# Kernel optimization log

Measured on AMD Instinct MI355X. Metric: run time of the kernel, lower is better.

Reference implementation:

```python
import jax, jax.numpy as jnp
import numpy as np
from jax.scipy.sparse.linalg import cg

SCALE = 8      # scaling_factor
CROP = 256     # crop_size
FEAT = 32      # per-branch feature channels
CG_ITERS = 100


def _conv(x, w, b):
    y = jax.lax.conv_general_dilated(x, w, (1, 1), 'SAME',
                                     dimension_numbers=('NCHW', 'OIHW', 'NCHW'))
    return y + b[None, :, None, None]


def _avgpool(x, r):
    B, C, H, W = x.shape
    return x.reshape(B, C, H // r, r, W // r, r).mean(axis=(3, 5))


def _up_adj(x, r):
    # adjoint of average-pool downsampling S: spread value / r^2 over the block
    return jnp.repeat(jnp.repeat(x, r, axis=2), r, axis=3) / (r * r)


def _features(guide, y_bicubic, gw1, gb1, gw2, gb2, sw1, sb1, sw2, sb2):
    g = _conv(jax.nn.relu(_conv(guide, gw1, gb1)), gw2, gb2)
    s = _conv(jax.nn.relu(_conv(y_bicubic, sw1, sb1)), sw2, sb2)
    return jnp.concatenate([g, s], axis=1)  # [B, 2*FEAT, H, W]


def _neighbor_affinity(f, mu, lam):
    # exp(-mu * ||f_i - f_j||^2) to the 4 grid neighbors, zero affinity at borders
    dv = jnp.sum((f[:, :, 1:, :] - f[:, :, :-1, :]) ** 2, axis=1)  # [B,H-1,W]
    dh = jnp.sum((f[:, :, :, 1:] - f[:, :, :, :-1]) ** 2, axis=1)  # [B,H,W-1]
    wv = jnp.exp(-mu * dv)
    wh = jnp.exp(-mu * dh)
    w_up = jnp.pad(wv, ((0, 0), (1, 0), (0, 0)))
    w_dn = jnp.pad(wv, ((0, 0), (0, 1), (0, 0)))
    w_lf = jnp.pad(wh, ((0, 0), (0, 0), (1, 0)))
    w_rt = jnp.pad(wh, ((0, 0), (0, 0), (0, 1)))
    deg = w_up + w_dn + w_lf + w_rt
    center = deg + lam  # diagonal of the system matrix (channel 4)
    return jnp.stack([w_up, w_dn, w_lf, w_rt, center], axis=1)  # [B,5,H,W]


def _graph_matvec(aff, mask_lr, lam, y):
    # A y = (D - W) y + lam * S^T M S y   (5-point graph Laplacian + LR data term)
    w_up, w_dn, w_lf, w_rt, center = (aff[:, i] for i in range(5))
    yy = y[:, 0]
    wy = (w_up * jnp.pad(yy[:, :-1, :], ((0, 0), (1, 0), (0, 0)))
          + w_dn * jnp.pad(yy[:, 1:, :], ((0, 0), (0, 1), (0, 0)))
          + w_lf * jnp.pad(yy[:, :, :-1], ((0, 0), (0, 0), (1, 0)))
          + w_rt * jnp.pad(yy[:, :, 1:], ((0, 0), (0, 0), (0, 1))))
    deg = center - lam
    lap = (deg * yy - wy)[:, None]
    data = lam * _up_adj(mask_lr * _avgpool(y, SCALE), SCALE)
    return lap + data


def setup_inputs() -> dict:
    key = jax.random.key(0)
    ks = jax.random.split(key, 20)
    B, H = 16, CROP
    r = SCALE
    w = lambda k, sh: jax.random.normal(k, sh, jnp.float32) * 0.05
    return {
        'guide': jax.random.normal(ks[0], (B, 3, H, H), jnp.float32),
        'source': jax.random.normal(ks[1], (B, 1, H // r, H // r), jnp.float32),
        'mask_lr': jnp.ones((B, 1, H // r, H // r), jnp.float32),
        'y_bicubic': jax.random.normal(ks[2], (B, 1, H, H), jnp.float32),
        # feature extractor (guide branch + source branch)
        'gw1': w(ks[3], (FEAT, 3, 3, 3)), 'gb1': jnp.zeros((FEAT,), jnp.float32),
        'gw2': w(ks[4], (FEAT, FEAT, 3, 3)), 'gb2': jnp.zeros((FEAT,), jnp.float32),
        'sw1': w(ks[5], (FEAT, 1, 3, 3)), 'sb1': jnp.zeros((FEAT,), jnp.float32),
        'sw2': w(ks[6], (FEAT, FEAT, 3, 3)), 'sb2': jnp.zeros((FEAT,), jnp.float32),
        # var_conv: VarEstimateModule(in=4, out=1, k=3)
        'vw1': w(ks[7], (FEAT, 4, 3, 3)), 'vb1': jnp.zeros((FEAT,), jnp.float32),
        'vw2': w(ks[8], (FEAT, FEAT, 3, 3)), 'vb2': jnp.zeros((FEAT,), jnp.float32),
        'vw3': w(ks[9], (1, FEAT, 3, 3)), 'vb3': jnp.zeros((1,), jnp.float32),
        # learned scalars (stored as log, as in the torch module)
        'log_lambda': jnp.log(jnp.array([1.0], jnp.float32)),
        'log_mu': jnp.log(jnp.array([0.1], jnp.float32)),
    }


def reference(guide, source, mask_lr, y_bicubic,
              gw1, gb1, gw2, gb2, sw1, sb1, sw2, sb2,
              vw1, vb1, vw2, vb2, vw3, vb3,
              log_lambda, log_mu):
    mu = jnp.exp(log_mu)[0]
    lam = jnp.exp(log_lambda)[0]
    # variance head on cat([guide, y_bicubic])
    v = jnp.concatenate([guide, y_bicubic], axis=1)
    v = jax.nn.relu(_conv(v, vw1, vb1))
    v = jax.nn.relu(_conv(v, vw2, vb2))
    var = _conv(v, vw3, vb3)
    # pixel affinities from multi-modal features
    feats = _features(guide, y_bicubic, gw1, gb1, gw2, gb2, sw1, sb1, sw2, sb2)
    aff = _neighbor_affinity(feats, mu, lam)
    # graph-regularised SR: solve (L + lam S^T M S) y = lam S^T (M source) by CG
    b = lam * _up_adj(mask_lr * source, SCALE)
    matvec = lambda y: _graph_matvec(aff, mask_lr, lam, y)
    y_pred, _ = cg(matvec, b, x0=y_bicubic, maxiter=CG_ITERS, tol=1e-6)
    return y_pred, var, aff
```

## Files before the change

### kernel.cpp

```cpp
#include <hip/hip_runtime.h>
#include <hip/hip_bf16.h>

typedef __hip_bfloat16 bf16;
typedef __attribute__((ext_vector_type(8))) short short8;
typedef __attribute__((ext_vector_type(4))) float f32x4;

#define NB 16
#define PLANE (256*256)

static __device__ __forceinline__ short f2bf(float v){
    __hip_bfloat16 h = __float2bfloat16(v);
    short s; __builtin_memcpy(&s, &h, 2); return s;
}
static __device__ __forceinline__ float bf2f(short s){
    union { unsigned u; float f; } cv;
    cv.u = ((unsigned)(unsigned short)s) << 16; return cv.f;
}

static __device__ __forceinline__ void  stg_ag(float* p, float v){
    __hip_atomic_store(p, v, __ATOMIC_RELAXED, __HIP_MEMORY_SCOPE_AGENT);
}
static __device__ __forceinline__ float ldg_ag(const float* p){
    return __hip_atomic_load(p, __ATOMIC_RELAXED, __HIP_MEMORY_SCOPE_AGENT);
}
static __device__ __forceinline__ void stg4_ag(float* p, f32x4 v){
    asm volatile("global_store_dwordx4 %0, %1, off sc0 sc1" :: "v"(p), "v"(v) : "memory");
}
static __device__ __forceinline__ f32x4 ldg4_ag(const float* p){
    f32x4 r;
    asm volatile("global_load_dwordx4 %0, %1, off sc0 sc1\n\ts_waitcnt vmcnt(0)"
                 : "=v"(r) : "v"(p) : "memory");
    return r;
}

template<int CIN, int SPLIT, bool RELU>
__global__ __launch_bounds__(256)
void conv3x3_first(const float* __restrict__ in, const float* __restrict__ in2,
                   const float* __restrict__ wgt, const float* __restrict__ bias,
                   bf16* __restrict__ out)
{
    __shared__ float s_in[CIN][18][18];
    __shared__ float s_w[CIN*9*32];
    const int n  = blockIdx.z;
    const int ty0 = blockIdx.y * 16, tx0 = blockIdx.x * 16;
    const int tid = threadIdx.x;

    for (int idx = tid; idx < CIN*9*32; idx += 256) {
        int co = idx & 31; int rest = idx >> 5;
        s_w[idx] = wgt[(co*CIN + rest/9)*9 + rest%9];
    }
    for (int idx = tid; idx < CIN*18*18; idx += 256) {
        int ci = idx / (18*18); int rr = idx % (18*18);
        int yy = rr / 18, xx = rr % 18;
        int y = ty0 + yy - 1, x = tx0 + xx - 1;
        float v = 0.f;
        if (y >= 0 && y < 256 && x >= 0 && x < 256) {
            if (ci < SPLIT) v = in [((size_t)(n*SPLIT + ci)*256 + y)*256 + x];
            else            v = in2[((size_t)(n*(CIN-SPLIT) + (ci-SPLIT))*256 + y)*256 + x];
        }
        s_in[ci][yy][xx] = v;
    }
    __syncthreads();

    const int ty = tid >> 4, tx = tid & 15;
    float acc[32];
    #pragma unroll
    for (int co = 0; co < 32; co++) acc[co] = bias[co];

    #pragma unroll
    for (int ci = 0; ci < CIN; ci++) {
        #pragma unroll
        for (int ky = 0; ky < 3; ky++)
        #pragma unroll
        for (int kx = 0; kx < 3; kx++) {
            float v = s_in[ci][ty+ky][tx+kx];
            const float* wp = &s_w[(ci*9 + ky*3 + kx)*32];
            #pragma unroll
            for (int co = 0; co < 32; co++) acc[co] = fmaf(v, wp[co], acc[co]);
        }
    }
    const int y = ty0 + ty, x = tx0 + tx;
    size_t base = (((size_t)n*256 + y)*256 + x)*32;
    #pragma unroll
    for (int c = 0; c < 32; c += 8) {
        short8 vv;
        #pragma unroll
        for (int j = 0; j < 8; j++) {
            float v = acc[c+j];
            if (RELU) v = fmaxf(v, 0.f);
            vv[j] = f2bf(v);
        }
        *(short8*)((short*)out + base + c) = vv;
    }
}

__global__ __launch_bounds__(256)
void wrepack3(const float* __restrict__ a, const float* __restrict__ b,
              const float* __restrict__ c,
              bf16* __restrict__ oa, bf16* __restrict__ ob, bf16* __restrict__ oc)
{
    int j = blockIdx.x*256 + threadIdx.x;
    if (j >= 3*9216) return;
    int set = j / 9216, r = j % 9216;
    int tap = r >> 10, rem = r & 1023, co = rem >> 5, ci = rem & 31;
    const float* src = (set == 0) ? a : (set == 1) ? b : c;
    bf16* dst = (set == 0) ? oa : (set == 1) ? ob : oc;
    dst[r] = __float2bfloat16(src[(co*32 + ci)*9 + tap]);
}

template<bool RELU>
__global__ __launch_bounds__(256)
void conv3x3_mfma(const bf16* __restrict__ in, const bf16* __restrict__ wpk,
                  const float* __restrict__ bias, bf16* __restrict__ out)
{
    __shared__ __align__(16) short s_a[4*2640];
    const int tid = threadIdx.x;
    const int lane = tid & 63, wid = tid >> 6;
    const int m = lane & 15, quad = lane >> 4, k0 = quad*8;
    const int n  = blockIdx.z;
    const int x0 = blockIdx.x * 16;
    const int y0 = blockIdx.y * 16;

    const short* inp = (const short*)in + (size_t)n*PLANE*32;
    short* outp = (short*)out + (size_t)n*PLANE*32;

    for (int c = tid; c < 1296; c += 256) {
        int q = c & 3, px = c >> 2;
        int yy = px / 18, xx = px - yy*18;
        int gy = y0 + yy - 1, gx = x0 + xx - 1;
        short8 v = {0,0,0,0,0,0,0,0};
        if ((unsigned)gy < 256u && (unsigned)gx < 256u)
            v = *(const short8*)(inp + ((size_t)(gy*256 + gx))*32 + q*8);
        *(short8*)(s_a + q*2640 + (yy*18 + xx)*8) = v;
    }

    const short* wp = (const short*)wpk;
    short8 bw[2][9];
    #pragma unroll
    for (int g = 0; g < 2; g++)
        #pragma unroll
        for (int tap = 0; tap < 9; tap++)
            bw[g][tap] = *(const short8*)(wp + ((tap*32 + g*16 + m)*32 + k0));
    const float b0 = bias[m], b1 = bias[16 + m];
    __syncthreads();

    const short* sa = s_a + quad*2640;
    #pragma unroll
    for (int r = 0; r < 4; r++) {
        const int lr = wid*4 + r;
        f32x4 acc0 = { b0, b0, b0, b0 };
        f32x4 acc1 = { b1, b1, b1, b1 };
        #pragma unroll
        for (int ky = 0; ky < 3; ky++)
        #pragma unroll
        for (int kx = 0; kx < 3; kx++) {
            short8 a = *(const short8*)(sa + ((lr+ky)*18 + (m+kx))*8);
            acc0 = __builtin_amdgcn_mfma_f32_16x16x32_bf16(a, bw[0][ky*3+kx], acc0, 0, 0, 0);
            acc1 = __builtin_amdgcn_mfma_f32_16x16x32_bf16(a, bw[1][ky*3+kx], acc1, 0, 0, 0);
        }
        const int y = y0 + lr;
        #pragma unroll
        for (int reg = 0; reg < 4; reg++) {
            int px = x0 + quad*4 + reg;
            size_t idx = ((size_t)y*256 + px)*32;
            float v0 = acc0[reg], v1 = acc1[reg];
            if (RELU) { v0 = fmaxf(v0, 0.f); v1 = fmaxf(v1, 0.f); }
            outp[idx + m]      = f2bf(v0);
            outp[idx + 16 + m] = f2bf(v1);
        }
    }
}

template<bool ACCUM>
__global__ __launch_bounds__(256, 2)
void conv3x3_mfma_dvdh(const bf16* __restrict__ in, const bf16* __restrict__ wpk,
                       const float* __restrict__ bias,
                       float* __restrict__ dv, float* __restrict__ dh)
{
    __shared__ __align__(16) short s_a[4*2896];
    __shared__ __align__(16) short s_f[17*17*40];
    const int tid = threadIdx.x;
    const int lane = tid & 63, wid = tid >> 6;
    const int m = lane & 15, quad = lane >> 4, k0 = quad*8;
    const int n  = blockIdx.z;
    const int x0 = blockIdx.x * 16;
    const int y0 = blockIdx.y * 16;

    const short* inp = (const short*)in + (size_t)n*PLANE*32;

    for (int c = tid; c < 1444; c += 256) {
        int q = c & 3, px = c >> 2;
        int yy = px / 19, xx = px - yy*19;
        int gy = y0 + yy - 1, gx = x0 + xx - 1;
        short8 v = {0,0,0,0,0,0,0,0};
        if ((unsigned)gy < 256u && (unsigned)gx < 256u)
            v = *(const short8*)(inp + ((size_t)(gy*256 + gx))*32 + q*8);
        *(short8*)(s_a + q*2896 + (yy*19 + xx)*8) = v;
    }

    const short* wp = (const short*)wpk;
    short8 bw[2][9];
    #pragma unroll
    for (int g = 0; g < 2; g++)
        #pragma unroll
        for (int tap = 0; tap < 9; tap++)
            bw[g][tap] = *(const short8*)(wp + ((tap*32 + g*16 + m)*32 + k0));
    const float b0 = bias[m], b1 = bias[16 + m];
    __syncthreads();

    const short* sa = s_a + quad*2896;

    for (int ru = 0; ru < 5; ru++) {
        const int yl = wid + 4*ru;
        if (yl > 16) break;
        f32x4 acc0 = { b0, b0, b0, b0 };
        f32x4 acc1 = { b1, b1, b1, b1 };
        #pragma unroll
        for (int ky = 0; ky < 3; ky++)
        #pragma unroll
        for (int kx = 0; kx < 3; kx++) {
            short8 a = *(const short8*)(sa + ((yl+ky)*19 + (kx+m))*8);
            acc0 = __builtin_amdgcn_mfma_f32_16x16x32_bf16(a, bw[0][ky*3+kx], acc0, 0, 0, 0);
            acc1 = __builtin_amdgcn_mfma_f32_16x16x32_bf16(a, bw[1][ky*3+kx], acc1, 0, 0, 0);
        }
        #pragma unroll
        for (int reg = 0; reg < 4; reg++) {
            int c = quad*4 + reg;
            short* fp = s_f + (yl*17 + c)*40;
            fp[m]      = f2bf(acc0[reg]);
            fp[16 + m] = f2bf(acc1[reg]);
        }
    }

    for (int ru = 0; ru < 4; ru++) {
        const int yl = wid + 4*ru;
        f32x4 acc0 = { b0, b0, b0, b0 };
        f32x4 acc1 = { b1, b1, b1, b1 };
        #pragma unroll
        for (int ky = 0; ky < 3; ky++)
        #pragma unroll
        for (int kx = 0; kx < 3; kx++) {
            int col = 16 + kx + m; if (col > 18) col = 18;
            short8 a = *(const short8*)(sa + ((yl+ky)*19 + col)*8);
            acc0 = __builtin_amdgcn_mfma_f32_16x16x32_bf16(a, bw[0][ky*3+kx], acc0, 0, 0, 0);
            acc1 = __builtin_amdgcn_mfma_f32_16x16x32_bf16(a, bw[1][ky*3+kx], acc1, 0, 0, 0);
        }
        if (quad == 0) {
            short* fp = s_f + (yl*17 + 16)*40;
            fp[m]      = f2bf(acc0[0]);
            fp[16 + m] = f2bf(acc1[0]);
        }
    }
    __syncthreads();

    const int ty = tid >> 4, tx = tid & 15;
    const int i = y0 + ty, j = x0 + tx;
    const short8* pc = (const short8*)(s_f + (ty*17 + tx)*40);
    const short8* pr = (j < 255) ? (const short8*)(s_f + (ty*17 + tx + 1)*40) : pc;
    const short8* pd = (i < 255) ? (const short8*)(s_f + ((ty+1)*17 + tx)*40) : pc;
    float adv = 0.f, adh = 0.f;
    #pragma unroll
    for (int c4 = 0; c4 < 4; c4++) {
        short8 sc = pc[c4], sr = pr[c4], sd = pd[c4];
        #pragma unroll
        for (int e = 0; e < 8; e++) {
            float fc = bf2f(sc[e]);
            float d1 = bf2f(sr[e]) - fc;
            float d2 = bf2f(sd[e]) - fc;
            adh = fmaf(d1, d1, adh);
            adv = fmaf(d2, d2, adv);
        }
    }
    int o = (n*256 + i)*256 + j;
    if (ACCUM) { dv[o] += adv; dh[o] += adh; }
    else       { dv[o]  = adv; dh[o]  = adh; }
}

__global__ __launch_bounds__(256)
void conv3x3_last(const bf16* __restrict__ in, const float* __restrict__ wgt,
                  const float* __restrict__ bias, float* __restrict__ out)
{
    __shared__ float s_w[288];
    int tid = threadIdx.x;
    for (int i = tid; i < 288; i += 256) s_w[i] = wgt[i];
    __syncthreads();
    int gid = blockIdx.x*256 + tid;
    int n = gid >> 16, h = (gid >> 8) & 255, w = gid & 255;
    const short* inp = (const short*)in + (size_t)n*PLANE*32;
    float sum = bias[0];
    #pragma unroll
    for (int ky = 0; ky < 3; ky++) {
        int yy = h + ky - 1;
        if ((unsigned)yy >= 256u) continue;
        #pragma unroll
        for (int kx = 0; kx < 3; kx++) {
            int xx = w + kx - 1;
            if ((unsigned)xx >= 256u) continue;
            const short8* pp = (const short8*)(inp + ((size_t)yy*256 + xx)*32);
            int tap = ky*3 + kx;
            #pragma unroll
            for (int c4 = 0; c4 < 4; c4++) {
                short8 v = pp[c4];
                #pragma unroll
                for (int j = 0; j < 8; j++)
                    sum = fmaf(bf2f(v[j]), s_w[(c4*8+j)*9 + tap], sum);
            }
        }
    }
    out[gid] = sum;
}

__global__ __launch_bounds__(256)
void aff2_kernel(const float* __restrict__ dv, const float* __restrict__ dh,
                 const float* __restrict__ llam, const float* __restrict__ lmu,
                 unsigned* __restrict__ wvh, float* __restrict__ aff)
{
    int bid = blockIdx.x;
    int n = bid >> 8, h = bid & 255, w = threadIdx.x;
    float mu = expf(lmu[0]), lam = expf(llam[0]);
    int rb = (n*256 + h)*256 + w;
    float wvv = (h < 255) ? expf(-mu * dv[rb]) : 0.f;
    float whv = (w < 255) ? expf(-mu * dh[rb]) : 0.f;
    unsigned pv = (unsigned)(unsigned short)f2bf(wvv);
    unsigned ph = (unsigned)(unsigned short)f2bf(whv);
    wvh[rb] = pv | (ph << 16);
    float w_up = (h > 0) ? expf(-mu * dv[rb - 256]) : 0.f;
    float w_lf = (w > 0) ? expf(-mu * dh[rb - 1])   : 0.f;
    float ctr  = w_up + wvv + w_lf + whv + lam;
    float* a = aff + ((size_t)n*5)*PLANE + h*256 + w;
    a[0]        = w_up;
    a[PLANE]    = wvv;
    a[2*PLANE]  = w_lf;
    a[3*PLANE]  = whv;
    a[4*PLANE]  = ctr;
}

__global__ __launch_bounds__(256, 2)
void cg_persist(const unsigned* __restrict__ wvh, const float* __restrict__ mask,
                const float* __restrict__ src, const float* __restrict__ ybic,
                const float* __restrict__ llam, float* __restrict__ xout,
                float* __restrict__ ebuf0, float* __restrict__ ebuf1,
                float* __restrict__ part4, float* __restrict__ res4)
{
    __shared__ float s_pn[66][34];
    __shared__ float s_part[256], s_bs[32];
    __shared__ float s_w3[12];
    __shared__ __align__(16) float s_g[16];

    const int tid = threadIdx.x;
    const int wb = blockIdx.x;
    const int n = wb >> 5, t = wb & 31;
    const int tyo = (t >> 3) * 64, txo = (t & 7) * 32;
    const int tx = tid & 31, tyb = tid >> 5;
    const int w = txo + tx;
    const float lam = expf(llam[0]);
    const bool is_leader = ((wb & 127) == 0);

    const unsigned* wn = wvh + (size_t)n*PLANE;
    const float* ybn = ybic + (size_t)n*PLANE;

    int idx[8];
    unsigned wc[8], wu[8], wl[8];
    float c1[8], rhs[8];
    #pragma unroll
    for (int i = 0; i < 8; i++) {
        int hhi = tyo + tyb + 8*i;
        idx[i] = hhi*256 + w;
        wc[i] = wn[idx[i]];
        wu[i] = (hhi > 0) ? wn[idx[i]-256] : 0u;
        wl[i] = (w > 0)   ? wn[idx[i]-1]   : 0u;
        int bi = n*1024 + (hhi>>3)*32 + (w>>3);
        float mv = mask[bi];
        c1[i]  = lam*mv*(1.f/4096.f);
        rhs[i] = lam*mv*src[bi]*(1.f/64.f);
    }

    const bool hthr = (tid < 192);
    int hy = 0, hx = 0; bool hin = false; int nb = 0, eoff = 0;
    if (hthr) {
        if      (tid < 32)  { hy = tyo - 1;         hx = txo + tid;
                              nb = wb - 8; eoff = 32 + tid; }
        else if (tid < 64)  { hy = tyo + 64;        hx = txo + (tid-32);
                              nb = wb + 8; eoff = tid - 32; }
        else if (tid < 128) { hy = tyo + (tid-64);  hx = txo - 1;
                              nb = wb - 1; eoff = 128 + (tid-64); }
        else                { hy = tyo + (tid-128); hx = txo + 32;
                              nb = wb + 1; eoff = 64 + (tid-128); }
        hin = (hy >= 0 && hy < 256 && hx >= 0 && hx < 256);
    }
    const int hsy = hy - tyo + 1, hsx = hx - txo + 1;

    #define POOL_BLOCK() do { \
        __syncthreads(); \
        { int segrow_ = tid >> 2, segcol_ = tid & 3; \
          const float* rw_ = &s_pn[1 + segrow_][1 + segcol_*8]; \
          s_part[tid] = rw_[0]+rw_[1]+rw_[2]+rw_[3]+rw_[4]+rw_[5]+rw_[6]+rw_[7]; } \
        __syncthreads(); \
        if (tid < 32) { int brow_ = tid >> 2, bcol_ = tid & 3; float s_ = 0.f; \
          _Pragma("unroll") \
          for (int rr_ = 0; rr_ < 8; rr_++) s_ += s_part[(brow_*8 + rr_)*4 + bcol_]; \
          s_bs[tid] = s_; } \
        __syncthreads(); \
    } while (0)

    #define PUBLISH_E(arr, ebase) do { \
        float* eb_ = (ebase) + (size_t)wb*192; \
        if (tyb == 0) stg_ag(eb_ + tx, arr[0]); \
        if (tyb == 7) stg_ag(eb_ + 32 + tx, arr[7]); \
        if (tx == 0) { _Pragma("unroll") \
            for (int i_ = 0; i_ < 8; i_++) stg_ag(eb_ + 64 + tyb + 8*i_, arr[i_]); } \
        if (tx == 31){ _Pragma("unroll") \
            for (int i_ = 0; i_ < 8; i_++) stg_ag(eb_ + 128 + tyb + 8*i_, arr[i_]); } \
    } while (0)

    auto matvec = [&](int i) -> float {
        int yy = 1 + tyb + 8*i, xx = 1 + tx;
        float wvd = bf2f((short)(wc[i] & 0xffff));
        float whr = bf2f((short)(wc[i] >> 16));
        float wvu = bf2f((short)(wu[i] & 0xffff));
        float whl = bf2f((short)(wl[i] >> 16));
        float s = wvu*s_pn[yy-1][xx] + wvd*s_pn[yy+1][xx]
                + whl*s_pn[yy][xx-1] + whr*s_pn[yy][xx+1];
        float deg = wvu+wvd+whl+whr;
        return deg*s_pn[yy][xx] - s + c1[i]*s_bs[i*4 + (tx>>3)];
    };

    auto publish_red = [&](unsigned seq, float va, float vb, float vc){
        #pragma unroll
        for (int o = 32; o > 0; o >>= 1) {
            va += __shfl_down(va, o, 64);
            vb += __shfl_down(vb, o, 64);
            vc += __shfl_down(vc, o, 64);
        }
        asm volatile("s_waitcnt vmcnt(0)" ::: "memory");
        __syncthreads();
        if ((tid & 63) == 0) { int wv = tid >> 6; s_w3[wv*3]=va; s_w3[wv*3+1]=vb; s_w3[wv*3+2]=vc; }
        __syncthreads();
        if (tid == 0) {
            f32x4 pk;
            pk[0] = s_w3[0]+s_w3[3]+s_w3[6]+s_w3[9];
            pk[1] = s_w3[1]+s_w3[4]+s_w3[7]+s_w3[10];
            pk[2] = s_w3[2]+s_w3[5]+s_w3[8]+s_w3[11];
            pk[3] = __uint_as_float(seq);
            stg4_ag(part4 + (size_t)((seq & 1)*512 + wb)*4, pk);
        }
    };

    float o0, o1, o2;
    auto allred = [&](unsigned seq){
        float* resp = res4 + (size_t)(seq & 1)*64;
        if (is_leader && tid < 64) {
            const float* pl = part4 + (size_t)(seq & 1)*2048;
            const float* p0 = pl + (size_t)(wb + 2*tid)*4;
            f32x4 a0 = ldg4_ag(p0);
            while (__float_as_uint(a0[3]) < seq) { __builtin_amdgcn_s_sleep(1); a0 = ldg4_ag(p0); }
            f32x4 a1 = ldg4_ag(p0 + 4);
            while (__float_as_uint(a1[3]) < seq) { __builtin_amdgcn_s_sleep(1); a1 = ldg4_ag(p0 + 4); }
            float pa = a0[0] + a1[0];
            float pb = a0[1] + a1[1];
            float pc = a0[2] + a1[2];
            #pragma unroll
            for (int o = 32; o > 0; o >>= 1) {
                pa += __shfl_down(pa, o, 64);
                pb += __shfl_down(pb, o, 64);
                pc += __shfl_down(pc, o, 64);
            }
            if (tid == 0) {
                f32x4 rk; rk[0] = pa; rk[1] = pb; rk[2] = pc; rk[3] = __uint_as_float(seq);
                stg4_ag(resp + (wb >> 7)*16, rk);
            }
        }
        if (tid < 4) {
            const float* rl = resp + tid*16;
            f32x4 g = ldg4_ag(rl);
            while (__float_as_uint(g[3]) < seq) { __builtin_amdgcn_s_sleep(2); g = ldg4_ag(rl); }
            *(f32x4*)&s_g[tid*4] = g;
        }
        __syncthreads();
        o0 = ((s_g[0]+s_g[4])+s_g[8])+s_g[12];
        o1 = ((s_g[1]+s_g[5])+s_g[9])+s_g[13];
        o2 = ((s_g[2]+s_g[6])+s_g[10])+s_g[14];
    };

    float xv[8], rv[8], pv[8], apv[8];
    float rh = 0.f, phh = 0.f;

    #pragma unroll
    for (int i = 0; i < 8; i++) {
        xv[i] = ybn[idx[i]];
        s_pn[1 + tyb + 8*i][1 + tx] = xv[i];
    }
    if (hthr) s_pn[hsy][hsx] = hin ? ybn[hy*256 + hx] : 0.f;
    POOL_BLOCK();
    float g0t = 0.f;
    #pragma unroll
    for (int i = 0; i < 8; i++) {
        float ax = matvec(i);
        float r0 = rhs[i] - ax;
        rv[i] = r0; pv[i] = r0;
        g0t += r0*r0;
    }
    PUBLISH_E(pv, ebuf1);
    publish_red(1u, 0.f, 0.f, 0.f);
    allred(1u);

    {
        float hv = 0.f;
        if (hthr && hin) hv = ldg_ag(ebuf1 + (size_t)nb*192 + eoff);
        if (hthr) { rh = hv; phh = hv; s_pn[hsy][hsx] = phh; }
        #pragma unroll
        for (int i = 0; i < 8; i++) s_pn[1 + tyb + 8*i][1 + tx] = pv[i];
        POOL_BLOCK();
        float pap = 0.f, apap = 0.f;
        #pragma unroll
        for (int i = 0; i < 8; i++) {
            float ap = matvec(i);
            apv[i] = ap;
            pap  += pv[i]*ap;
            apap += ap*ap;
        }
        PUBLISH_E(apv, ebuf0);
        publish_red(2u, g0t, pap, apap);
    }

    for (int k = 1; k <= 99; k++) {
        float* ebR = ((k+1) & 1) ? ebuf1 : ebuf0;
        float* ebW = ((k+2) & 1) ? ebuf1 : ebuf0;

        allred((unsigned)(k + 1));
        float alpha = o0 / o1;
        float beta  = (alpha*alpha*o2 - o0) / o0;

        float hv = 0.f;
        if (hthr && hin) hv = ldg_ag(ebR + (size_t)nb*192 + eoff);

        float gsum = 0.f;
        #pragma unroll
        for (int i = 0; i < 8; i++) {
            float rN = fmaf(-alpha, apv[i], rv[i]);
            xv[i] = fmaf(alpha, pv[i], xv[i]);
            float pN = fmaf(beta, pv[i], rN);
            rv[i] = rN; pv[i] = pN;
            gsum += rN*rN;
            s_pn[1 + tyb + 8*i][1 + tx] = pN;
        }
        if (hthr) {
            rh  = fmaf(-alpha, hv, rh);
            phh = fmaf(beta, phh, rh);
            s_pn[hsy][hsx] = phh;
        }
        POOL_BLOCK();
        float pap = 0.f, apap = 0.f;
        #pragma unroll
        for (int i = 0; i < 8; i++) {
            float ap = matvec(i);
            apv[i] = ap;
            pap  += pv[i]*ap;
            apap += ap*ap;
        }
        PUBLISH_E(apv, ebW);
        publish_red((unsigned)(k + 2), gsum, pap, apap);
    }

    allred(101u);
    float alphaT = o0 / o1;
    float* xn = xout + (size_t)n*PLANE;
    #pragma unroll
    for (int i = 0; i < 8; i++) xn[idx[i]] = fmaf(alphaT, pv[i], xv[i]);

    #undef POOL_BLOCK
    #undef PUBLISH_E
}

extern "C" void kernel_launch(void* const* d_in, const int* in_sizes, int n_in,
                              void* d_out, int out_size, void* d_ws, size_t ws_size,
                              hipStream_t stream)
{
    (void)in_sizes; (void)n_in; (void)out_size; (void)ws_size;
    const float* guide = (const float*)d_in[0];
    const float* source= (const float*)d_in[1];
    const float* mask  = (const float*)d_in[2];
    const float* ybic  = (const float*)d_in[3];
    const float* gw1 = (const float*)d_in[4];  const float* gb1 = (const float*)d_in[5];
    const float* gw2 = (const float*)d_in[6];  const float* gb2 = (const float*)d_in[7];
    const float* sw1 = (const float*)d_in[8];  const float* sb1 = (const float*)d_in[9];
    const float* sw2 = (const float*)d_in[10]; const float* sb2 = (const float*)d_in[11];
    const float* vw1 = (const float*)d_in[12]; const float* vb1 = (const float*)d_in[13];
    const float* vw2 = (const float*)d_in[14]; const float* vb2 = (const float*)d_in[15];
    const float* vw3 = (const float*)d_in[16]; const float* vb3 = (const float*)d_in[17];
    const float* llam = (const float*)d_in[18];
    const float* lmu  = (const float*)d_in[19];

    float* out     = (float*)d_out;
    float* x_out   = out;
    float* var_out = out + 1048576;
    float* aff_out = out + 2097152;

    char* ws = (char*)d_ws;
    float*    res4  = (float*)ws;
    float*    part4 = (float*)(ws + 4096);
    bf16*     wpk1  = (bf16*)(ws + 24576);
    bf16*     wpk2  = (bf16*)(ws + 43008);
    bf16*     wpk3  = (bf16*)(ws + 61440);
    unsigned* wvh   = (unsigned*)(ws + 131072);
    char*     A     = ws + 131072 + (size_t)NB*PLANE*4;
    bf16*  tmp1 = (bf16*)(A);
    bf16*  tmp2 = (bf16*)(A + (size_t)NB*32*PLANE*2);
    float* dv   = (float*)(A + (size_t)NB*32*PLANE*4);
    float* dh   = (float*)(A + (size_t)NB*32*PLANE*4 + (size_t)NB*PLANE*4);
    float* ebuf0 = (float*)A;
    float* ebuf1 = (float*)(A + (size_t)512*192*4);

    dim3 cgrid(16, 16, NB);

    hipMemsetAsync(ws, 0, 20480, stream);

    wrepack3<<<108,256,0,stream>>>(gw2, sw2, vw2, wpk1, wpk2, wpk3);

    conv3x3_first<3,3,true><<<cgrid,256,0,stream>>>(guide, guide, gw1, gb1, tmp1);
    conv3x3_mfma_dvdh<false><<<cgrid,256,0,stream>>>(tmp1, wpk1, gb2, dv, dh);
    conv3x3_first<1,1,true><<<cgrid,256,0,stream>>>(ybic, ybic, sw1, sb1, tmp1);
    conv3x3_mfma_dvdh<true><<<cgrid,256,0,stream>>>(tmp1, wpk2, sb2, dv, dh);
    aff2_kernel<<<4096,256,0,stream>>>(dv, dh, llam, lmu, wvh, aff_out);
    conv3x3_first<4,3,true><<<cgrid,256,0,stream>>>(guide, ybic, vw1, vb1, tmp1);
    conv3x3_mfma<true><<<cgrid,256,0,stream>>>(tmp1, wpk3, vb2, tmp2);
    conv3x3_last<<<4096,256,0,stream>>>(tmp2, vw3, vb3, var_out);

    cg_persist<<<512,256,0,stream>>>(wvh, mask, source, ybic, llam, x_out,
                                     ebuf0, ebuf1, part4, res4);
}
```

Measured before the change: 894.5 us.

## Fuse both feature-branch second convs, dv/dh, and affinity into one kernel

Both feature branches' second 3x3 convolutions, the squared-difference sums and the exp affinity computation now run in one kernel, with dv/dh kept in shared memory. This removes the global dv/dh round trips, the read-modify-write accumulation pass and the separate aff2 launch. In exchange, each tile recomputes a halo of 18x18 conv outputs (from 17x17) so the up/left neighbours are available locally, and shared-memory use per block rises. The first-layer outputs of the two branches now go to separate buffers.

Result: slower. 986.0 us (+10.2%).

```diff
diff --git a/kernel.cpp b/kernel.cpp
--- a/kernel.cpp
+++ b/kernel.cpp
@@ -171,14 +171,17 @@
     }
 }
 
-template<bool ACCUM>
 __global__ __launch_bounds__(256, 2)
-void conv3x3_mfma_dvdh(const bf16* __restrict__ in, const bf16* __restrict__ wpk,
-                       const float* __restrict__ bias,
-                       float* __restrict__ dv, float* __restrict__ dh)
+void featfuse(const bf16* __restrict__ ing, const bf16* __restrict__ ins,
+              const bf16* __restrict__ wpk1, const float* __restrict__ gb2,
+              const bf16* __restrict__ wpk2, const float* __restrict__ sb2,
+              const float* __restrict__ llam, const float* __restrict__ lmu,
+              unsigned* __restrict__ wvh, float* __restrict__ aff)
 {
-    __shared__ __align__(16) short s_a[4*2896];
-    __shared__ __align__(16) short s_f[17*17*40];
+    __shared__ __align__(16) short s_a[4*3248];
+    __shared__ __align__(16) short s_f[18*18*40];
+    __shared__ float s_dv[17][17], s_dh[17][17];
+
     const int tid = threadIdx.x;
     const int lane = tid & 63, wid = tid >> 6;
     const int m = lane & 15, quad = lane >> 4, k0 = quad*8;
@@ -186,94 +189,127 @@
     const int x0 = blockIdx.x * 16;
     const int y0 = blockIdx.y * 16;
 
-    const short* inp = (const short*)in + (size_t)n*PLANE*32;
-
-    for (int c = tid; c < 1444; c += 256) {
-        int q = c & 3, px = c >> 2;
-        int yy = px / 19, xx = px - yy*19;
-        int gy = y0 + yy - 1, gx = x0 + xx - 1;
-        short8 v = {0,0,0,0,0,0,0,0};
-        if ((unsigned)gy < 256u && (unsigned)gx < 256u)
-            v = *(const short8*)(inp + ((size_t)(gy*256 + gx))*32 + q*8);
-        *(short8*)(s_a + q*2896 + (yy*19 + xx)*8) = v;
-    }
-
-    const short* wp = (const short*)wpk;
-    short8 bw[2][9];
-    #pragma unroll
-    for (int g = 0; g < 2; g++)
-        #pragma unroll
-        for (int tap = 0; tap < 9; tap++)
-            bw[g][tap] = *(const short8*)(wp + ((tap*32 + g*16 + m)*32 + k0));
-    const float b0 = bias[m], b1 = bias[16 + m];
-    __syncthreads();
-
-    const short* sa = s_a + quad*2896;
-
-    for (int ru = 0; ru < 5; ru++) {
-        const int yl = wid + 4*ru;
-        if (yl > 16) break;
-        f32x4 acc0 = { b0, b0, b0, b0 };
-        f32x4 acc1 = { b1, b1, b1, b1 };
-        #pragma unroll
-        for (int ky = 0; ky < 3; ky++)
-        #pragma unroll
-        for (int kx = 0; kx < 3; kx++) {
-            short8 a = *(const short8*)(sa + ((yl+ky)*19 + (kx+m))*8);
-            acc0 = __builtin_amdgcn_mfma_f32_16x16x32_bf16(a, bw[0][ky*3+kx], acc0, 0, 0, 0);
-            acc1 = __builtin_amdgcn_mfma_f32_16x16x32_bf16(a, bw[1][ky*3+kx], acc1, 0, 0, 0);
-        }
-        #pragma unroll
-        for (int reg = 0; reg < 4; reg++) {
-            int c = quad*4 + reg;
-            short* fp = s_f + (yl*17 + c)*40;
-            fp[m]      = f2bf(acc0[reg]);
-            fp[16 + m] = f2bf(acc1[reg]);
-        }
-    }
-
-    for (int ru = 0; ru < 4; ru++) {
-        const int yl = wid + 4*ru;
-        f32x4 acc0 = { b0, b0, b0, b0 };
-        f32x4 acc1 = { b1, b1, b1, b1 };
-        #pragma unroll
-        for (int ky = 0; ky < 3; ky++)
-        #pragma unroll
-        for (int kx = 0; kx < 3; kx++) {
-            int col = 16 + kx + m; if (col > 18) col = 18;
-            short8 a = *(const short8*)(sa + ((yl+ky)*19 + col)*8);
-            acc0 = __builtin_amdgcn_mfma_f32_16x16x32_bf16(a, bw[0][ky*3+kx], acc0, 0, 0, 0);
-            acc1 = __builtin_amdgcn_mfma_f32_16x16x32_bf16(a, bw[1][ky*3+kx], acc1, 0, 0, 0);
-        }
-        if (quad == 0) {
-            short* fp = s_f + (yl*17 + 16)*40;
-            fp[m]      = f2bf(acc0[0]);
-            fp[16 + m] = f2bf(acc1[0]);
-        }
-    }
+    auto stage20 = [&](const short* inp){
+        for (int c = tid; c < 1600; c += 256) {
+            int q = c & 3, px = c >> 2;
+            int yy = px / 20, xx = px - yy*20;
+            int gy = y0 + yy - 2, gx = x0 + xx - 2;
+            short8 v = {0,0,0,0,0,0,0,0};
+            if ((unsigned)gy < 256u && (unsigned)gx < 256u)
+                v = *(const short8*)(inp + ((size_t)(gy*256 + gx))*32 + q*8);
+            *(short8*)(s_a + q*3248 + (yy*20 + xx)*8) = v;
+        }
+    };
+
+    auto conv2 = [&](const bf16* wpk, const float* bias){
+        const short* wp = (const short*)wpk;
+        short8 bw[2][9];
+        #pragma unroll
+        for (int g = 0; g < 2; g++)
+            #pragma unroll
+            for (int tap = 0; tap < 9; tap++)
+                bw[g][tap] = *(const short8*)(wp + ((tap*32 + g*16 + m)*32 + k0));
+        const float b0 = bias[m], b1 = bias[16 + m];
+        const short* sa = s_a + quad*3248;
+
+        for (int ly = wid; ly < 18; ly += 4) {
+            f32x4 acc0 = { b0, b0, b0, b0 };
+            f32x4 acc1 = { b1, b1, b1, b1 };
+            #pragma unroll
+            for (int ky = 0; ky < 3; ky++)
+            #pragma unroll
+            for (int kx = 0; kx < 3; kx++) {
+                short8 a = *(const short8*)(sa + ((ly+ky)*20 + (m+kx))*8);
+                acc0 = __builtin_amdgcn_mfma_f32_16x16x32_bf16(a, bw[0][ky*3+kx], acc0, 0, 0, 0);
+                acc1 = __builtin_amdgcn_mfma_f32_16x16x32_bf16(a, bw[1][ky*3+kx], acc1, 0, 0, 0);
+            }
+            #pragma unroll
+            for (int reg = 0; reg < 4; reg++) {
+                int lx = quad*4 + reg;
+                short* fp = s_f + (ly*18 + lx)*40;
+                fp[m]      = f2bf(acc0[reg]);
+                fp[16 + m] = f2bf(acc1[reg]);
+            }
+            f32x4 e0 = { b0, b0, b0, b0 };
+            f32x4 e1 = { b1, b1, b1, b1 };
+            #pragma unroll
+            for (int ky = 0; ky < 3; ky++)
+            #pragma unroll
+            for (int kx = 0; kx < 3; kx++) {
+                int col = 16 + m + kx; if (col > 19) col = 19;
+                short8 a = *(const short8*)(sa + ((ly+ky)*20 + col)*8);
+                e0 = __builtin_amdgcn_mfma_f32_16x16x32_bf16(a, bw[0][ky*3+kx], e0, 0, 0, 0);
+                e1 = __builtin_amdgcn_mfma_f32_16x16x32_bf16(a, bw[1][ky*3+kx], e1, 0, 0, 0);
+            }
+            if (quad == 0) {
+                #pragma unroll
+                for (int reg = 0; reg < 2; reg++) {
+                    short* fp = s_f + (ly*18 + 16 + reg)*40;
+                    fp[m]      = f2bf(e0[reg]);
+                    fp[16 + m] = f2bf(e1[reg]);
+                }
+            }
+        }
+    };
+
+    auto dvdh = [&](bool accum){
+        for (int p = tid; p < 289; p += 256) {
+            int li = p / 17, lj = p % 17;
+            int gi = y0 - 1 + li, gj = x0 - 1 + lj;
+            const short8* pc = (const short8*)(s_f + (li*18 + lj)*40);
+            const short8* pr = (gj < 255) ? (const short8*)(s_f + (li*18 + lj + 1)*40) : pc;
+            const short8* pd = (gi < 255) ? (const short8*)(s_f + ((li+1)*18 + lj)*40) : pc;
+            float adv = 0.f, adh = 0.f;
+            #pragma unroll
+            for (int c4 = 0; c4 < 4; c4++) {
+                short8 sc = pc[c4], sr = pr[c4], sd = pd[c4];
+                #pragma unroll
+                for (int e = 0; e < 8; e++) {
+                    float fc = bf2f(sc[e]);
+                    float d1 = bf2f(sr[e]) - fc;
+                    float d2 = bf2f(sd[e]) - fc;
+                    adh = fmaf(d1, d1, adh);
+                    adv = fmaf(d2, d2, adv);
+                }
+            }
+            if (accum) { s_dv[li][lj] += adv; s_dh[li][lj] += adh; }
+            else       { s_dv[li][lj]  = adv; s_dh[li][lj]  = adh; }
+        }
+    };
+
+    const short* ipg = (const short*)ing + (size_t)n*PLANE*32;
+    const short* ips = (const short*)ins + (size_t)n*PLANE*32;
+
+    stage20(ipg);
+    __syncthreads();
+    conv2(wpk1, gb2);
+    __syncthreads();
+    dvdh(false);
+    stage20(ips);
+    __syncthreads();
+    conv2(wpk2, sb2);
+    __syncthreads();
+    dvdh(true);
     __syncthreads();
 
     const int ty = tid >> 4, tx = tid & 15;
-    const int i = y0 + ty, j = x0 + tx;
-    const short8* pc = (const short8*)(s_f + (ty*17 + tx)*40);
-    const short8* pr = (j < 255) ? (const short8*)(s_f + (ty*17 + tx + 1)*40) : pc;
-    const short8* pd = (i < 255) ? (const short8*)(s_f + ((ty+1)*17 + tx)*40) : pc;
-    float adv = 0.f, adh = 0.f;
-    #pragma unroll
-    for (int c4 = 0; c4 < 4; c4++) {
-        short8 sc = pc[c4], sr = pr[c4], sd = pd[c4];
-        #pragma unroll
-        for (int e = 0; e < 8; e++) {
-            float fc = bf2f(sc[e]);
-            float d1 = bf2f(sr[e]) - fc;
-            float d2 = bf2f(sd[e]) - fc;
-            adh = fmaf(d1, d1, adh);
-            adv = fmaf(d2, d2, adv);
-        }
-    }
-    int o = (n*256 + i)*256 + j;
-    if (ACCUM) { dv[o] += adv; dh[o] += adh; }
-    else       { dv[o]  = adv; dh[o]  = adh; }
+    const int h = y0 + ty, w = x0 + tx;
+    const float mu = expf(lmu[0]), lam = expf(llam[0]);
+    int rb = (n*256 + h)*256 + w;
+    float wvv = (h < 255) ? expf(-mu * s_dv[ty+1][tx+1]) : 0.f;
+    float whv = (w < 255) ? expf(-mu * s_dh[ty+1][tx+1]) : 0.f;
+    unsigned pv = (unsigned)(unsigned short)f2bf(wvv);
+    unsigned ph = (unsigned)(unsigned short)f2bf(whv);
+    wvh[rb] = pv | (ph << 16);
+    float w_up = (h > 0) ? expf(-mu * s_dv[ty][tx+1]) : 0.f;
+    float w_lf = (w > 0) ? expf(-mu * s_dh[ty+1][tx]) : 0.f;
+    float ctr  = w_up + wvv + w_lf + whv + lam;
+    float* a = aff + ((size_t)n*5)*PLANE + h*256 + w;
+    a[0]        = w_up;
+    a[PLANE]    = wvv;
+    a[2*PLANE]  = w_lf;
+    a[3*PLANE]  = whv;
+    a[4*PLANE]  = ctr;
 }
 
 __global__ __launch_bounds__(256)
@@ -308,31 +344,6 @@
         }
     }
     out[gid] = sum;
-}
-
-__global__ __launch_bounds__(256)
-void aff2_kernel(const float* __restrict__ dv, const float* __restrict__ dh,
-                 const float* __restrict__ llam, const float* __restrict__ lmu,
-                 unsigned* __restrict__ wvh, float* __restrict__ aff)
-{
-    int bid = blockIdx.x;
-    int n = bid >> 8, h = bid & 255, w = threadIdx.x;
-    float mu = expf(lmu[0]), lam = expf(llam[0]);
-    int rb = (n*256 + h)*256 + w;
-    float wvv = (h < 255) ? expf(-mu * dv[rb]) : 0.f;
-    float whv = (w < 255) ? expf(-mu * dh[rb]) : 0.f;
-    unsigned pv = (unsigned)(unsigned short)f2bf(wvv);
-    unsigned ph = (unsigned)(unsigned short)f2bf(whv);
-    wvh[rb] = pv | (ph << 16);
-    float w_up = (h > 0) ? expf(-mu * dv[rb - 256]) : 0.f;
-    float w_lf = (w > 0) ? expf(-mu * dh[rb - 1])   : 0.f;
-    float ctr  = w_up + wvv + w_lf + whv + lam;
-    float* a = aff + ((size_t)n*5)*PLANE + h*256 + w;
-    a[0]        = w_up;
-    a[PLANE]    = wvv;
-    a[2*PLANE]  = w_lf;
-    a[3*PLANE]  = whv;
-    a[4*PLANE]  = ctr;
 }
 
 __global__ __launch_bounds__(256, 2)
@@ -604,10 +615,8 @@
     bf16*     wpk3  = (bf16*)(ws + 61440);
     unsigned* wvh   = (unsigned*)(ws + 131072);
     char*     A     = ws + 131072 + (size_t)NB*PLANE*4;
-    bf16*  tmp1 = (bf16*)(A);
-    bf16*  tmp2 = (bf16*)(A + (size_t)NB*32*PLANE*2);
-    float* dv   = (float*)(A + (size_t)NB*32*PLANE*4);
-    float* dh   = (float*)(A + (size_t)NB*32*PLANE*4 + (size_t)NB*PLANE*4);
+    bf16*  tmpA = (bf16*)(A);
+    bf16*  tmpB = (bf16*)(A + (size_t)NB*32*PLANE*2);
     float* ebuf0 = (float*)A;
     float* ebuf1 = (float*)(A + (size_t)512*192*4);
 
@@ -617,14 +626,13 @@
 
     wrepack3<<<108,256,0,stream>>>(gw2, sw2, vw2, wpk1, wpk2, wpk3);
 
-    conv3x3_first<3,3,true><<<cgrid,256,0,stream>>>(guide, guide, gw1, gb1, tmp1);
-    conv3x3_mfma_dvdh<false><<<cgrid,256,0,stream>>>(tmp1, wpk1, gb2, dv, dh);
-    conv3x3_first<1,1,true><<<cgrid,256,0,stream>>>(ybic, ybic, sw1, sb1, tmp1);
-    conv3x3_mfma_dvdh<true><<<cgrid,256,0,stream>>>(tmp1, wpk2, sb2, dv, dh);
-    aff2_kernel<<<4096,256,0,stream>>>(dv, dh, llam, lmu, wvh, aff_out);
-    conv3x3_first<4,3,true><<<cgrid,256,0,stream>>>(guide, ybic, vw1, vb1, tmp1);
-    conv3x3_mfma<true><<<cgrid,256,0,stream>>>(tmp1, wpk3, vb2, tmp2);
-    conv3x3_last<<<4096,256,0,stream>>>(tmp2, vw3, vb3, var_out);
+    conv3x3_first<3,3,true><<<cgrid,256,0,stream>>>(guide, guide, gw1, gb1, tmpA);
+    conv3x3_first<1,1,true><<<cgrid,256,0,stream>>>(ybic, ybic, sw1, sb1, tmpB);
+    featfuse<<<cgrid,256,0,stream>>>(tmpA, tmpB, wpk1, gb2, wpk2, sb2,
+                                     llam, lmu, wvh, aff_out);
+    conv3x3_first<4,3,true><<<cgrid,256,0,stream>>>(guide, ybic, vw1, vb1, tmpA);
+    conv3x3_mfma<true><<<cgrid,256,0,stream>>>(tmpA, wpk3, vb2, tmpB);
+    conv3x3_last<<<4096,256,0,stream>>>(tmpB, vw3, vb3, var_out);
 
     cg_persist<<<512,256,0,stream>>>(wvh, mask, source, ybic, llam, x_out,
                                      ebuf0, ebuf1, part4, res4);
```

## Merge guide/source branch convs into shared launches and fuse variance conv1 with affinity

Applied to the files above, without the earlier changes.

Runs the guide and source first-layer convs in one launch, and their MFMA second-layer convs with dv/dh reduction in one launch, using a doubled z-grid. The two branches' dv/dh contributions now combine through atomicAdd into a buffer cleared beforehand, instead of a write pass followed by an accumulate pass. The variance head's first conv shares one launch with the affinity kernel through block-index partitioning. This cuts the number of launches and serialization points and gives each launch more blocks, at the cost of an extra memset and float atomics.

Measured after the change: 876.0 us. -2.1%, faster.

```diff
diff --git a/kernel.cpp b/kernel.cpp
--- a/kernel.cpp
+++ b/kernel.cpp
@@ -33,24 +33,19 @@
     return r;
 }
 
-template<int CIN, int SPLIT, bool RELU>
-__global__ __launch_bounds__(256)
-void conv3x3_first(const float* __restrict__ in, const float* __restrict__ in2,
-                   const float* __restrict__ wgt, const float* __restrict__ bias,
-                   bf16* __restrict__ out)
-{
-    __shared__ float s_in[CIN][18][18];
-    __shared__ float s_w[CIN*9*32];
-    const int n  = blockIdx.z;
-    const int ty0 = blockIdx.y * 16, tx0 = blockIdx.x * 16;
-    const int tid = threadIdx.x;
-
+template<int CIN, int SPLIT>
+static __device__ __forceinline__ void conv1_body(
+    const float* __restrict__ in, const float* __restrict__ in2,
+    const float* __restrict__ wgt, const float* __restrict__ bias,
+    bf16* __restrict__ out, float* s_in, float* s_w,
+    int n, int ty0, int tx0, int tid)
+{
     for (int idx = tid; idx < CIN*9*32; idx += 256) {
         int co = idx & 31; int rest = idx >> 5;
         s_w[idx] = wgt[(co*CIN + rest/9)*9 + rest%9];
     }
     for (int idx = tid; idx < CIN*18*18; idx += 256) {
-        int ci = idx / (18*18); int rr = idx % (18*18);
+        int ci = idx / 324; int rr = idx % 324;
         int yy = rr / 18, xx = rr % 18;
         int y = ty0 + yy - 1, x = tx0 + xx - 1;
         float v = 0.f;
@@ -58,7 +53,7 @@
             if (ci < SPLIT) v = in [((size_t)(n*SPLIT + ci)*256 + y)*256 + x];
             else            v = in2[((size_t)(n*(CIN-SPLIT) + (ci-SPLIT))*256 + y)*256 + x];
         }
-        s_in[ci][yy][xx] = v;
+        s_in[ci*324 + yy*18 + xx] = v;
     }
     __syncthreads();
 
@@ -73,7 +68,7 @@
         for (int ky = 0; ky < 3; ky++)
         #pragma unroll
         for (int kx = 0; kx < 3; kx++) {
-            float v = s_in[ci][ty+ky][tx+kx];
+            float v = s_in[ci*324 + (ty+ky)*18 + (tx+kx)];
             const float* wp = &s_w[(ci*9 + ky*3 + kx)*32];
             #pragma unroll
             for (int co = 0; co < 32; co++) acc[co] = fmaf(v, wp[co], acc[co]);
@@ -85,13 +80,27 @@
     for (int c = 0; c < 32; c += 8) {
         short8 vv;
         #pragma unroll
-        for (int j = 0; j < 8; j++) {
-            float v = acc[c+j];
-            if (RELU) v = fmaxf(v, 0.f);
-            vv[j] = f2bf(v);
-        }
+        for (int j = 0; j < 8; j++)
+            vv[j] = f2bf(fmaxf(acc[c+j], 0.f));
         *(short8*)((short*)out + base + c) = vv;
     }
+}
+
+__global__ __launch_bounds__(256)
+void conv1_gs(const float* __restrict__ guide, const float* __restrict__ ybic,
+              const float* __restrict__ gw1, const float* __restrict__ gb1,
+              const float* __restrict__ sw1, const float* __restrict__ sb1,
+              bf16* __restrict__ outg, bf16* __restrict__ outs)
+{
+    __shared__ float s_in[3*324];
+    __shared__ float s_w[3*9*32];
+    const int zz = blockIdx.z;
+    const int br = zz >> 4, n = zz & 15;
+    const int ty0 = blockIdx.y * 16, tx0 = blockIdx.x * 16;
+    if (br == 0)
+        conv1_body<3,3>(guide, guide, gw1, gb1, outg, s_in, s_w, n, ty0, tx0, threadIdx.x);
+    else
+        conv1_body<1,1>(ybic, ybic, sw1, sb1, outs, s_in, s_w, n, ty0, tx0, threadIdx.x);
 }
 
 __global__ __launch_bounds__(256)
@@ -171,20 +180,25 @@
     }
 }
 
-template<bool ACCUM>
 __global__ __launch_bounds__(256, 2)
-void conv3x3_mfma_dvdh(const bf16* __restrict__ in, const bf16* __restrict__ wpk,
-                       const float* __restrict__ bias,
-                       float* __restrict__ dv, float* __restrict__ dh)
+void conv2gs_dvdh(const bf16* __restrict__ ing, const bf16* __restrict__ ins,
+                  const bf16* __restrict__ wpk1, const float* __restrict__ gb2,
+                  const bf16* __restrict__ wpk2, const float* __restrict__ sb2,
+                  float* __restrict__ dv, float* __restrict__ dh)
 {
     __shared__ __align__(16) short s_a[4*2896];
     __shared__ __align__(16) short s_f[17*17*40];
     const int tid = threadIdx.x;
     const int lane = tid & 63, wid = tid >> 6;
     const int m = lane & 15, quad = lane >> 4, k0 = quad*8;
-    const int n  = blockIdx.z;
+    const int zz = blockIdx.z;
+    const int br = zz >> 4, n = zz & 15;
     const int x0 = blockIdx.x * 16;
     const int y0 = blockIdx.y * 16;
+
+    const bf16* in = br ? ins : ing;
+    const bf16* wpk = br ? wpk2 : wpk1;
+    const float* bias = br ? sb2 : gb2;
 
     const short* inp = (const short*)in + (size_t)n*PLANE*32;
 
@@ -272,8 +286,8 @@
         }
     }
     int o = (n*256 + i)*256 + j;
-    if (ACCUM) { dv[o] += adv; dh[o] += adh; }
-    else       { dv[o]  = adv; dh[o]  = adh; }
+    atomicAdd(&dv[o], adv);
+    atomicAdd(&dh[o], adh);
 }
 
 __global__ __launch_bounds__(256)
@@ -311,11 +325,23 @@
 }
 
 __global__ __launch_bounds__(256)
-void aff2_kernel(const float* __restrict__ dv, const float* __restrict__ dh,
-                 const float* __restrict__ llam, const float* __restrict__ lmu,
-                 unsigned* __restrict__ wvh, float* __restrict__ aff)
-{
-    int bid = blockIdx.x;
+void conv1v_aff(const float* __restrict__ guide, const float* __restrict__ ybic,
+                const float* __restrict__ vw1, const float* __restrict__ vb1,
+                bf16* __restrict__ outv,
+                const float* __restrict__ dv, const float* __restrict__ dh,
+                const float* __restrict__ llam, const float* __restrict__ lmu,
+                unsigned* __restrict__ wvh, float* __restrict__ aff)
+{
+    __shared__ float s_in[4*324];
+    __shared__ float s_w[4*9*32];
+    const int b = blockIdx.x;
+    if (b < 4096) {
+        int n = b >> 8, by = (b >> 4) & 15, bx = b & 15;
+        conv1_body<4,3>(guide, ybic, vw1, vb1, outv, s_in, s_w,
+                        n, by*16, bx*16, threadIdx.x);
+        return;
+    }
+    int bid = b - 4096;
     int n = bid >> 8, h = bid & 255, w = threadIdx.x;
     float mu = expf(lmu[0]), lam = expf(llam[0]);
     int rb = (n*256 + h)*256 + w;
@@ -604,27 +630,26 @@
     bf16*     wpk3  = (bf16*)(ws + 61440);
     unsigned* wvh   = (unsigned*)(ws + 131072);
     char*     A     = ws + 131072 + (size_t)NB*PLANE*4;
-    bf16*  tmp1 = (bf16*)(A);
-    bf16*  tmp2 = (bf16*)(A + (size_t)NB*32*PLANE*2);
+    bf16*  tmpA = (bf16*)(A);
+    bf16*  tmpB = (bf16*)(A + (size_t)NB*32*PLANE*2);
     float* dv   = (float*)(A + (size_t)NB*32*PLANE*4);
     float* dh   = (float*)(A + (size_t)NB*32*PLANE*4 + (size_t)NB*PLANE*4);
     float* ebuf0 = (float*)A;
     float* ebuf1 = (float*)(A + (size_t)512*192*4);
 
-    dim3 cgrid(16, 16, NB);
-
     hipMemsetAsync(ws, 0, 20480, stream);
+    hipMemsetAsync(dv, 0, (size_t)2*NB*PLANE*4, stream);
 
     wrepack3<<<108,256,0,stream>>>(gw2, sw2, vw2, wpk1, wpk2, wpk3);
 
-    conv3x3_first<3,3,true><<<cgrid,256,0,stream>>>(guide, guide, gw1, gb1, tmp1);
-    conv3x3_mfma_dvdh<false><<<cgrid,256,0,stream>>>(tmp1, wpk1, gb2, dv, dh);
-    conv3x3_first<1,1,true><<<cgrid,256,0,stream>>>(ybic, ybic, sw1, sb1, tmp1);
-    conv3x3_mfma_dvdh<true><<<cgrid,256,0,stream>>>(tmp1, wpk2, sb2, dv, dh);
-    aff2_kernel<<<4096,256,0,stream>>>(dv, dh, llam, lmu, wvh, aff_out);
-    conv3x3_first<4,3,true><<<cgrid,256,0,stream>>>(guide, ybic, vw1, vb1, tmp1);
-    conv3x3_mfma<true><<<cgrid,256,0,stream>>>(tmp1, wpk3, vb2, tmp2);
-    conv3x3_last<<<4096,256,0,stream>>>(tmp2, vw3, vb3, var_out);
+    conv1_gs<<<dim3(16,16,2*NB),256,0,stream>>>(guide, ybic, gw1, gb1, sw1, sb1,
+                                                tmpA, tmpB);
+    conv2gs_dvdh<<<dim3(16,16,2*NB),256,0,stream>>>(tmpA, tmpB, wpk1, gb2, wpk2, sb2,
+                                                    dv, dh);
+    conv1v_aff<<<8192,256,0,stream>>>(guide, ybic, vw1, vb1, tmpA,
+                                      dv, dh, llam, lmu, wvh, aff_out);
+    conv3x3_mfma<true><<<dim3(16,16,NB),256,0,stream>>>(tmpA, wpk3, vb2, tmpB);
+    conv3x3_last<<<4096,256,0,stream>>>(tmpB, vw3, vb3, var_out);
 
     cg_persist<<<512,256,0,stream>>>(wvh, mask, source, ybic, llam, x_out,
                                      ebuf0, ebuf1, part4, res4);
```
